# Optimization experiments

Measured on AMD Instinct MI355X. Metric: run time of the kernel, lower is better.

The kernel has to match this reference:

```python
import jax, jax.numpy as jnp
import numpy as np

N_NODES = 10000
N_EDGES = 320000
N_REL = 460
N_BASES = 30
D = 200


def setup_inputs() -> dict:
    key = jax.random.key(0)
    k = jax.random.split(key, 8)
    x = jax.random.normal(k[0], (N_NODES, D), dtype=jnp.float32)
    edge_index = jax.random.randint(k[1], (2, N_EDGES), 0, N_NODES, dtype=jnp.int32)
    edge_type = jax.random.randint(k[2], (N_EDGES,), 0, N_REL, dtype=jnp.int32)
    # Xavier-uniform-like init scales
    w_bound = float(np.sqrt(6.0 / (D + D)))
    c_bound = float(np.sqrt(6.0 / (N_REL + N_BASES)))
    weight = jax.random.uniform(k[3], (N_BASES, D, D), minval=-w_bound, maxval=w_bound, dtype=jnp.float32)
    coeff = jax.random.uniform(k[4], (N_REL, N_BASES), minval=-c_bound, maxval=c_bound, dtype=jnp.float32)
    self_weight = jax.random.uniform(k[5], (D, D), minval=-w_bound, maxval=w_bound, dtype=jnp.float32)
    bias = jnp.zeros((D,), dtype=jnp.float32)
    return {
        "x": x,
        "weight": weight,
        "coeff": coeff,
        "self_weight": self_weight,
        "bias": bias,
        "edge_index": edge_index,
        "edge_type": edge_type,
        "num_nodes": N_NODES,
    }


def reference(x, weight, coeff, self_weight, bias, edge_index, edge_type, num_nodes):
    # RelationalGraphConv.forward:
    #   W_r = sum_b coeff[r, b] * V_b ; msg_e = x[src_e] @ W_{type_e}
    #   out[n] = (sum_{e: tgt_e = n} msg_e) / max(in_deg[n], 1) + x @ W_self + bias
    src = edge_index[0]
    tgt = edge_index[1]
    src_feats = x[src]                    # (E, d_in) gather
    edge_coeff = coeff[edge_type]         # (E, B) gather

    # msg_e = sum_b coeff[type_e, b] * (src_e @ V_b): scan over bases to avoid
    # materializing an (E, B, d_out) intermediate (same math as W_r = coeff @ V).
    def body(acc, inputs):
        Vb, cb = inputs                   # (d_in, d_out), (E,)
        return acc + (src_feats @ Vb) * cb[:, None], None

    msg0 = jnp.zeros((src.shape[0], weight.shape[2]), dtype=x.dtype)
    msg, _ = jax.lax.scan(body, msg0, (weight, edge_coeff.T))  # (E, d_out)

    out = jax.ops.segment_sum(msg, tgt, num_segments=num_nodes)              # (N, d_out)
    deg = jax.ops.segment_sum(jnp.ones_like(tgt, dtype=x.dtype), tgt, num_segments=num_nodes)
    out = out / jnp.clip(deg, 1.0)[:, None]
    out = out + x @ self_weight + bias
    return out
```

## Files before the change

kernel.cpp:

```cpp
#include <hip/hip_runtime.h>
#include <hip/hip_bf16.h>

#define N_NODES 10000
#define N_EDGES 320000
#define N_REL   460
#define N_BASES 30
#define DIM     200
#define KZ      6016
#define KT      6240
#define NSTEPS  195
#define NTILES  157
#define NFRAG   16
#define KSPLIT  6
#define PROWS   10048
#define TKELEM  2048

#define PREP_B8 (NFRAG * NSTEPS * 64)
#define PREP_C  (N_REL * 16)
#define PREP_X8 (N_NODES * 28)
#define S1_TOTAL (N_EDGES + PREP_B8 + PREP_C)
#define S2_TOTAL (N_EDGES + PREP_X8)

using short8  = __attribute__((ext_vector_type(8))) short;
using s4v     = __attribute__((ext_vector_type(4))) short;
using floatx4 = __attribute__((ext_vector_type(4))) float;

__device__ __forceinline__ unsigned short f2bf(float f) {
    union { float f; unsigned u; } v; v.f = f;
    unsigned u = v.u;
    return (unsigned short)((u + 0x7fffu + ((u >> 16) & 1u)) >> 16);
}

__device__ __forceinline__ short8 pack8(const unsigned short* u) {
    union { unsigned short s[8]; short8 v; } p;
#pragma unroll
    for (int i = 0; i < 8; ++i) p.s[i] = u[i];
    return p.v;
}

__device__ __forceinline__ size_t asw_idx(int n, int c) {
    int t = n >> 6, sub = (n >> 4) & 3, rl = n & 15;
    int kk = c >> 5, w = c & 31;
    return (size_t)(t * NSTEPS + kk) * TKELEM + sub * 512 + rl * 32 + w;
}


__global__ void sort1_kernel(const int* __restrict__ tgt, int* __restrict__ deg,
                             const float* __restrict__ weight, const float* __restrict__ sw,
                             const float* __restrict__ coeff,
                             unsigned short* __restrict__ BSW, unsigned int* __restrict__ Cpair) {
    int idx = blockIdx.x * blockDim.x + threadIdx.x;
    if (idx < N_EDGES) {
        atomicAdd(&deg[tgt[idx]], 1);
        return;
    }
    idx -= N_EDGES;
    if (idx < PREP_B8) {
        int f = idx / (NSTEPS * 64);
        int rem = idx - f * (NSTEPS * 64);
        int kk = rem >> 6;
        int l = rem & 63;
        int rB = f * 16 + (l & 15);
        int kbase = kk * 32 + (l >> 4) * 8;
        unsigned short bs[8];
#pragma unroll
        for (int j = 0; j < 8; ++j) {
            int k = kbase + j;
            float v = 0.f;
            if (rB < DIM) {
                if (k < KZ) {
                    if (k < N_BASES * DIM) {
                        int b = k / DIM, kc = k - b * DIM;
                        v = weight[(b * DIM + kc) * DIM + rB];
                    }
                } else {
                    int jj = k - KZ;
                    if (jj < DIM) v = sw[jj * DIM + rB];
                }
            }
            bs[j] = f2bf(v);
        }
        *(short8*)(BSW + (size_t)idx * 8) = pack8(bs);
        return;
    }
    idx -= PREP_B8;
    if (idx < PREP_C) {
        int t = idx >> 4, m = idx & 15;
        unsigned lo = f2bf(coeff[t * N_BASES + m]);
        unsigned hi = (m + 16 < N_BASES) ? f2bf(coeff[t * N_BASES + m + 16]) : 0u;
        Cpair[idx] = lo | (hi << 16);
    }
}

__global__ __launch_bounds__(1024) void scan_kernel(const int* deg, int* starts,
                                                    int* cursor, float* dinv) {
    __shared__ int part[1024];
    int tid = threadIdx.x;
    const int PER = (N_NODES + 1023) / 1024;
    int base = tid * PER;
    int s = 0;
    for (int i = 0; i < PER; ++i) { int idx = base + i; if (idx < N_NODES) s += deg[idx]; }
    part[tid] = s; __syncthreads();
    for (int off = 1; off < 1024; off <<= 1) {
        int v = (tid >= off) ? part[tid - off] : 0;
        __syncthreads();
        part[tid] += v;
        __syncthreads();
    }
    int run = (tid > 0) ? part[tid - 1] : 0;
    for (int i = 0; i < PER; ++i) {
        int idx = base + i;
        if (idx < N_NODES) {
            int d = deg[idx];
            starts[idx] = run; cursor[idx] = run;
            dinv[idx] = 1.0f / (float)(d > 0 ? d : 1);
            run += d;
        }
    }
    if (tid == 1023) starts[N_NODES] = part[1023];
}


__global__ void sort2_kernel(const int* __restrict__ src, const int* __restrict__ tgt,
                             const int* __restrict__ etype, int* __restrict__ cursor,
                             int2* __restrict__ sedge,
                             const float* __restrict__ x, const int* __restrict__ deg,
                             unsigned short* __restrict__ XbfP, unsigned short* __restrict__ ASW) {
    int idx = blockIdx.x * blockDim.x + threadIdx.x;
    if (idx < N_EDGES) {
        int t = tgt[idx];
        int pos = atomicAdd(&cursor[t], 1);
        sedge[pos] = make_int2(src[idx], etype[idx]);
        return;
    }
    idx -= N_EDGES;
    if (idx < PREP_X8) {
        int n = idx / 28, t = idx - n * 28;
        int p = t >> 2, c4 = (t & 3) << 2;
        int cl = p * 32 + c4;
        int ch = cl + 16;
        int d = deg[n]; if (d < 1) d = 1;
        float df = (float)d;
        floatx4 vlo = (floatx4){0.f, 0.f, 0.f, 0.f};
        floatx4 vhi = (floatx4){0.f, 0.f, 0.f, 0.f};
        if (cl < DIM) vlo = *(const floatx4*)(x + (size_t)n * DIM + cl);
        if (ch < DIM) vhi = *(const floatx4*)(x + (size_t)n * DIM + ch);
        unsigned short xp[8], asl[4], ash[4];
#pragma unroll
        for (int i = 0; i < 4; ++i) {
            xp[2 * i]     = f2bf(vlo[i]);
            xp[2 * i + 1] = f2bf(vhi[i]);
            asl[i] = f2bf(df * vlo[i]);
            ash[i] = f2bf(df * vhi[i]);
        }
        *(short8*)(XbfP + (size_t)n * 224 + p * 32 + c4 * 2) = pack8(xp);
        union { unsigned short s[4]; s4v v; } ul, uh;
#pragma unroll
        for (int i = 0; i < 4; ++i) { ul.s[i] = asl[i]; uh.s[i] = ash[i]; }
        *(s4v*)(ASW + asw_idx(n, KZ + cl)) = ul.v;
        *(s4v*)(ASW + asw_idx(n, KZ + ch)) = uh.v;
    }
}


__global__ __launch_bounds__(256) void agg_kernel(const unsigned int* __restrict__ XbfP,
                                                  const unsigned int* __restrict__ Cpair,
                                                  const int* __restrict__ starts,
                                                  const int2* __restrict__ sedge,
                                                  unsigned short* __restrict__ ASW) {
    __shared__ __align__(16) unsigned short zbuf[4][3232];
    int lane = threadIdx.x & 63;
    int wave = threadIdx.x >> 6;
    int n = blockIdx.x * 4 + wave;
    int ln = lane & 15, q = lane >> 4;

    floatx4 acc0[13], acc1[13];
#pragma unroll
    for (int f = 0; f < 13; ++f) {
        acc0[f] = (floatx4){0.f, 0.f, 0.f, 0.f};
        acc1[f] = acc0[f];
    }

    int e0 = starts[n], e1 = starts[n + 1];
    for (int kb = e0; kb < e1; kb += 32) {
        int eb = kb + 8 * q;
        unsigned short a0v[8], a1v[8];
        int srcs[8];
#pragma unroll
        for (int j = 0; j < 8; ++j) {
            int e = eb + j;
            int ec = (e < e1) ? e : (e1 - 1);
            int2 sd = sedge[ec];
            unsigned cp = (e < e1) ? Cpair[sd.y * 16 + ln] : 0u;
            a0v[j] = (unsigned short)(cp & 0xffffu);
            a1v[j] = (unsigned short)(cp >> 16);
            srcs[j] = sd.x;
        }
        short8 A0 = pack8(a0v), A1 = pack8(a1v);

        unsigned pv[2][8];
#pragma unroll
        for (int j = 0; j < 8; ++j)
            pv[0][j] = XbfP[(size_t)srcs[j] * 112 + ln];
#pragma unroll
        for (int p = 0; p < 7; ++p) {
            int cur = p & 1, nxt = cur ^ 1;
            if (p < 6) {
#pragma unroll
                for (int j = 0; j < 8; ++j)
                    pv[nxt][j] = XbfP[(size_t)srcs[j] * 112 + (p + 1) * 16 + ln];
            }
            unsigned short lo[8], hi[8];
#pragma unroll
            for (int j = 0; j < 8; ++j) {
                lo[j] = (unsigned short)(pv[cur][j] & 0xffffu);
                hi[j] = (unsigned short)(pv[cur][j] >> 16);
            }
            short8 Blo = pack8(lo), Bhi = pack8(hi);
            int f0 = 2 * p;
            acc0[f0] = __builtin_amdgcn_mfma_f32_16x16x32_bf16(A0, Blo, acc0[f0], 0, 0, 0);
            acc1[f0] = __builtin_amdgcn_mfma_f32_16x16x32_bf16(A1, Blo, acc1[f0], 0, 0, 0);
            if (2 * p + 1 < 13) {
                acc0[2 * p + 1] = __builtin_amdgcn_mfma_f32_16x16x32_bf16(A0, Bhi, acc0[2 * p + 1], 0, 0, 0);
                acc1[2 * p + 1] = __builtin_amdgcn_mfma_f32_16x16x32_bf16(A1, Bhi, acc1[2 * p + 1], 0, 0, 0);
            }
        }
    }

    unsigned short* zb = zbuf[wave];
    int t = n >> 6, sub = (n >> 4) & 3, rl = n & 15;
    const uint4* zb4 = (const uint4*)zb;
    uint4* dst = (uint4*)ASW;
    size_t base_u4 = (size_t)t * NSTEPS * 256 + sub * 64 + rl * 4;

#pragma unroll
    for (int f = 0; f < 13; ++f) {
        int d = f * 16 + ln;
        if (d < DIM) {
#pragma unroll
            for (int i = 0; i < 4; ++i)
                zb[(q * 4 + i) * DIM + d] = f2bf(acc0[f][i]);
        }
    }
    for (int v = lane; v < 400; v += 64) {
        int kk = v >> 2, w8 = v & 3;
        dst[base_u4 + (size_t)kk * 256 + w8] = zb4[v];
    }

    if (lane < 16) zb[2800 + lane] = 0;
#pragma unroll
    for (int f = 0; f < 13; ++f) {
        int d = f * 16 + ln;
        if (d < DIM) {
#pragma unroll
            for (int i = 0; i < 4; ++i) {
                int b1 = 16 + q * 4 + i;
                if (b1 < N_BASES) zb[(b1 - 16) * DIM + d] = f2bf(acc1[f][i]);
            }
        }
    }
    for (int v = lane; v < 352; v += 64) {
        int kk = 100 + (v >> 2), w8 = v & 3;
        dst[base_u4 + (size_t)kk * 256 + w8] = zb4[v];
    }
}


#define GITER(VLIT, BU, BL, KK)                                                        \
  {                                                                                    \
    asm volatile("s_waitcnt vmcnt(" #VLIT ")" ::: "memory");                           \
    __builtin_amdgcn_sched_barrier(0);                                                 \
    asm volatile("s_barrier" ::: "memory");                                            \
    const int kk_ = (KK);                                                              \
    const int kld_ = (kk_ + 1 < ke) ? kk_ + 1 : ke - 1;                                \
    BL[0] = *(const short8*)(pb + ((size_t)(0 * 4 * NSTEPS) + kld_) * 512);            \
    BL[1] = *(const short8*)(pb + ((size_t)(1 * 4 * NSTEPS) + kld_) * 512);            \
    BL[2] = *(const short8*)(pb + ((size_t)(2 * 4 * NSTEPS) + kld_) * 512);            \
    BL[3] = *(const short8*)(pb + ((size_t)(3 * 4 * NSTEPS) + kld_) * 512);            \
    const int kst_ = (kk_ + 7 < ke) ? kk_ + 7 : ke - 1;                                \
    __builtin_amdgcn_global_load_lds(                                                  \
        (const unsigned int*)(aswt + (size_t)kst_ * TKELEM + goff),                    \
        (unsigned int*)(ldsw + ((kk_ + 7) & 7) * 2048), 16, 0, 0);                     \
    const unsigned short* sp_ = alds + (kk_ & 7) * 2048 + pread8;                      \
    short8 av0 = *(const short8*)(sp_);                                                \
    short8 av1 = *(const short8*)(sp_ + 512);                                          \
    short8 av2 = *(const short8*)(sp_ + 1024);                                         \
    short8 av3 = *(const short8*)(sp_ + 1536);                                         \
    _Pragma("unroll")                                                                  \
    for (int i_ = 0; i_ < 4; ++i_) {                                                   \
      acc[i_][0] = __builtin_amdgcn_mfma_f32_16x16x32_bf16(av0, BU[i_], acc[i_][0], 0, 0, 0); \
      acc[i_][1] = __builtin_amdgcn_mfma_f32_16x16x32_bf16(av1, BU[i_], acc[i_][1], 0, 0, 0); \
      acc[i_][2] = __builtin_amdgcn_mfma_f32_16x16x32_bf16(av2, BU[i_], acc[i_][2], 0, 0, 0); \
      acc[i_][3] = __builtin_amdgcn_mfma_f32_16x16x32_bf16(av3, BU[i_], acc[i_][3], 0, 0, 0); \
    }                                                                                  \
  }

__global__ __launch_bounds__(256, 4) void gemm_kernel(const unsigned short* __restrict__ ASW,
                                                      const unsigned short* __restrict__ BSW,
                                                      float* __restrict__ part) {
    __shared__ __align__(16) unsigned short alds[8 * 2048];
    int tid = threadIdx.x;
    int lane = tid & 63, wave = tid >> 6;
    int tile = blockIdx.x, chunk = blockIdx.y;
    int ks = (chunk * NSTEPS) / KSPLIT;
    int ke = ((chunk + 1) * NSTEPS) / KSPLIT;
    int ln = lane & 15, q = lane >> 4;

    const unsigned short* aswt = ASW + (size_t)tile * NSTEPS * TKELEM;
    const unsigned short* pb = BSW + (size_t)(wave * NSTEPS) * 512 + lane * 8;

    int gsw = (tid & 0xE0) | ((tid & 7) << 2) | ((tid >> 3) & 3);
    int goff = gsw * 8;
    int pread8 = ((((ln >> 3) & 1) << 5) | (q << 3) | (ln & 7)) * 8;
    unsigned short* ldsw = alds + wave * 512;

    floatx4 acc[4][4];
#pragma unroll
    for (int i = 0; i < 4; ++i)
#pragma unroll
        for (int s = 0; s < 4; ++s) acc[i][s] = (floatx4){0.f, 0.f, 0.f, 0.f};

    short8 bA[4], bB[4];

#pragma unroll
    for (int i = 0; i < 4; ++i)
        bA[i] = *(const short8*)(pb + ((size_t)(i * 4 * NSTEPS) + ks) * 512);
#pragma unroll
    for (int d = 0; d < 7; ++d)
        __builtin_amdgcn_global_load_lds(
            (const unsigned int*)(aswt + (size_t)(ks + d) * TKELEM + goff),
            (unsigned int*)(ldsw + ((ks + d) & 7) * 2048), 16, 0, 0);

    GITER(0,  bA, bB, ks + 0);
    GITER(5,  bB, bA, ks + 1);
    GITER(10, bA, bB, ks + 2);
    GITER(15, bB, bA, ks + 3);
    GITER(20, bA, bB, ks + 4);
    GITER(25, bB, bA, ks + 5);

    int kk = ks + 6;
    for (; kk + 1 < ke; kk += 2) {
        GITER(30, bA, bB, kk);
        GITER(30, bB, bA, kk + 1);
    }
    if (kk < ke) { GITER(30, bA, bB, kk); }

    int row0 = tile * 64;
    float* pbase = part + ((size_t)chunk * PROWS + row0) * 208;
#pragma unroll
    for (int i = 0; i < 4; ++i) {
        int fg = wave + 4 * i;
        if (fg < 13) {
            int c = fg * 16 + ln;
#pragma unroll
            for (int s = 0; s < 4; ++s)
#pragma unroll
                for (int ii = 0; ii < 4; ++ii)
                    pbase[(s * 16 + q * 4 + ii) * 208 + c] = acc[i][s][ii];
        }
    }
}


__global__ __launch_bounds__(256) void reduce_kernel(const float* __restrict__ part,
                                                     const float* __restrict__ dinv,
                                                     const float* __restrict__ bias,
                                                     float* __restrict__ out) {
    int idx = blockIdx.x * blockDim.x + threadIdx.x;
    if (idx >= N_NODES * 50) return;
    int r = idx / 50, cq = idx - r * 50;
    float4 s = {0.f, 0.f, 0.f, 0.f};
#pragma unroll
    for (int c = 0; c < KSPLIT; ++c) {
        float4 v = *(const float4*)(part + ((size_t)c * PROWS + r) * 208 + cq * 4);
        s.x += v.x; s.y += v.y; s.z += v.z; s.w += v.w;
    }
    float dv = dinv[r];
    float4 b = *(const float4*)(bias + cq * 4);
    float4 o;
    o.x = s.x * dv + b.x; o.y = s.y * dv + b.y;
    o.z = s.z * dv + b.z; o.w = s.w * dv + b.w;
    *(float4*)(out + (size_t)r * DIM + cq * 4) = o;
}


extern "C" void kernel_launch(void* const* d_in, const int* in_sizes, int n_in,
                              void* d_out, int out_size, void* d_ws, size_t ws_size,
                              hipStream_t stream) {
    const float* x      = (const float*)d_in[0];
    const float* weight = (const float*)d_in[1];
    const float* coeff  = (const float*)d_in[2];
    const float* selfw  = (const float*)d_in[3];
    const float* bias   = (const float*)d_in[4];
    const int*   eidx   = (const int*)d_in[5];
    const int*   etype  = (const int*)d_in[6];
    const int* src = eidx;
    const int* tgt = eidx + N_EDGES;
    float* out = (float*)d_out;

    char* ws = (char*)d_ws;
    size_t off = 0;
    auto carve = [&](size_t bytes) {
        char* p = ws + off;
        off += (bytes + 255) & ~(size_t)255;
        return p;
    };
    unsigned short* ASW  = (unsigned short*)carve((size_t)NTILES * NSTEPS * TKELEM * 2);
    unsigned short* BSW  = (unsigned short*)carve((size_t)NFRAG * NSTEPS * 512 * 2);
    float* part   = (float*)carve((size_t)KSPLIT * PROWS * 208 * 4);
    unsigned short* XbfP = (unsigned short*)carve((size_t)(N_NODES * 224 + 64) * 2);
    unsigned int*  Cpair = (unsigned int*)carve((size_t)N_REL * 16 * 4);
    int*   deg    = (int*)carve((size_t)N_NODES * 4);
    int*   starts = (int*)carve((size_t)(N_NODES + 1) * 4);
    int*   cursor = (int*)carve((size_t)N_NODES * 4);
    float* dinv   = (float*)carve((size_t)N_NODES * 4);
    int2*  sedge  = (int2*)carve((size_t)N_EDGES * 8);

    hipMemsetAsync(deg, 0, (size_t)N_NODES * 4, stream);

    sort1_kernel<<<(S1_TOTAL + 255) / 256, 256, 0, stream>>>(
        tgt, deg, weight, selfw, coeff, BSW, Cpair);

    scan_kernel<<<1, 1024, 0, stream>>>(deg, starts, cursor, dinv);

    sort2_kernel<<<(S2_TOTAL + 255) / 256, 256, 0, stream>>>(
        src, tgt, etype, cursor, sedge, x, deg, XbfP, ASW);

    agg_kernel<<<N_NODES / 4, 256, 0, stream>>>(
        (const unsigned int*)XbfP, Cpair, starts, sedge, ASW);

    dim3 ggrid(NTILES, KSPLIT);
    gemm_kernel<<<ggrid, 256, 0, stream>>>(ASW, BSW, part);

    reduce_kernel<<<(N_NODES * 50 + 255) / 256, 256, 0, stream>>>(part, dinv, bias, out);
}
```

Measured before the change: 254.7 us.

## Fuse memset, degree count, scan and edge sort into one cooperative kernel

Replaces the memset plus three separate preprocessing kernels (degree count/weight prep, prefix scan, edge bucketing/x prep) with a single cooperative kernel of 512 blocks that uses grid-wide syncs between phases. The aim is to remove several kernel launches and their inter-kernel gaps. In exchange, the scan now runs on 256 threads inside block 0 while every other block waits at the grid barrier. Grid-stride loops with a fixed grid may also use the machine less fully than the earlier one-thread-per-item launches.

```diff
diff --git a/kernel.cpp b/kernel.cpp
--- a/kernel.cpp
+++ b/kernel.cpp
@@ -1,5 +1,8 @@
 #include <hip/hip_runtime.h>
 #include <hip/hip_bf16.h>
+#include <hip/hip_cooperative_groups.h>
+
+namespace cg = cooperative_groups;
 
 #define N_NODES 10000
 #define N_EDGES 320000
@@ -18,8 +21,6 @@
 #define PREP_B8 (NFRAG * NSTEPS * 64)
 #define PREP_C  (N_REL * 16)
 #define PREP_X8 (N_NODES * 28)
-#define S1_TOTAL (N_EDGES + PREP_B8 + PREP_C)
-#define S2_TOTAL (N_EDGES + PREP_X8)
 
 using short8  = __attribute__((ext_vector_type(8))) short;
 using s4v     = __attribute__((ext_vector_type(4))) short;
@@ -45,19 +46,26 @@
 }
 
 
-__global__ void sort1_kernel(const int* __restrict__ tgt, int* __restrict__ deg,
-                             const float* __restrict__ weight, const float* __restrict__ sw,
-                             const float* __restrict__ coeff,
-                             unsigned short* __restrict__ BSW, unsigned int* __restrict__ Cpair) {
-    int idx = blockIdx.x * blockDim.x + threadIdx.x;
-    if (idx < N_EDGES) {
-        atomicAdd(&deg[tgt[idx]], 1);
-        return;
-    }
-    idx -= N_EDGES;
-    if (idx < PREP_B8) {
-        int f = idx / (NSTEPS * 64);
-        int rem = idx - f * (NSTEPS * 64);
+__global__ __launch_bounds__(256) void fused_sort_kernel(
+    const int* __restrict__ src, const int* __restrict__ tgt,
+    const int* __restrict__ etype,
+    const float* __restrict__ x, const float* __restrict__ weight,
+    const float* __restrict__ sw, const float* __restrict__ coeff,
+    int* deg, int* starts, int* cursor, float* dinv, int2* sedge,
+    unsigned short* __restrict__ XbfP, unsigned short* __restrict__ ASW,
+    unsigned short* __restrict__ BSW, unsigned int* __restrict__ Cpair)
+{
+    cg::grid_group grid = cg::this_grid();
+    int gsz = gridDim.x * blockDim.x;
+    int gid = blockIdx.x * blockDim.x + threadIdx.x;
+
+    for (int i = gid; i < N_NODES; i += gsz) deg[i] = 0;
+    grid.sync();
+
+    for (int i = gid; i < N_EDGES; i += gsz) atomicAdd(&deg[tgt[i]], 1);
+    for (int i = gid; i < PREP_B8; i += gsz) {
+        int f = i / (NSTEPS * 64);
+        int rem = i - f * (NSTEPS * 64);
         int kk = rem >> 6;
         int l = rem & 63;
         int rB = f * 16 + (l & 15);
@@ -80,62 +88,51 @@
             }
             bs[j] = f2bf(v);
         }
-        *(short8*)(BSW + (size_t)idx * 8) = pack8(bs);
-        return;
-    }
-    idx -= PREP_B8;
-    if (idx < PREP_C) {
-        int t = idx >> 4, m = idx & 15;
+        *(short8*)(BSW + (size_t)i * 8) = pack8(bs);
+    }
+    for (int i = gid; i < PREP_C; i += gsz) {
+        int t = i >> 4, m = i & 15;
         unsigned lo = f2bf(coeff[t * N_BASES + m]);
         unsigned hi = (m + 16 < N_BASES) ? f2bf(coeff[t * N_BASES + m + 16]) : 0u;
-        Cpair[idx] = lo | (hi << 16);
-    }
-}
-
-__global__ __launch_bounds__(1024) void scan_kernel(const int* deg, int* starts,
-                                                    int* cursor, float* dinv) {
-    __shared__ int part[1024];
-    int tid = threadIdx.x;
-    const int PER = (N_NODES + 1023) / 1024;
-    int base = tid * PER;
-    int s = 0;
-    for (int i = 0; i < PER; ++i) { int idx = base + i; if (idx < N_NODES) s += deg[idx]; }
-    part[tid] = s; __syncthreads();
-    for (int off = 1; off < 1024; off <<= 1) {
-        int v = (tid >= off) ? part[tid - off] : 0;
-        __syncthreads();
-        part[tid] += v;
-        __syncthreads();
-    }
-    int run = (tid > 0) ? part[tid - 1] : 0;
-    for (int i = 0; i < PER; ++i) {
-        int idx = base + i;
-        if (idx < N_NODES) {
-            int d = deg[idx];
-            starts[idx] = run; cursor[idx] = run;
-            dinv[idx] = 1.0f / (float)(d > 0 ? d : 1);
-            run += d;
-        }
-    }
-    if (tid == 1023) starts[N_NODES] = part[1023];
-}
-
-
-__global__ void sort2_kernel(const int* __restrict__ src, const int* __restrict__ tgt,
-                             const int* __restrict__ etype, int* __restrict__ cursor,
-                             int2* __restrict__ sedge,
-                             const float* __restrict__ x, const int* __restrict__ deg,
-                             unsigned short* __restrict__ XbfP, unsigned short* __restrict__ ASW) {
-    int idx = blockIdx.x * blockDim.x + threadIdx.x;
-    if (idx < N_EDGES) {
-        int t = tgt[idx];
+        Cpair[i] = lo | (hi << 16);
+    }
+    grid.sync();
+
+    if (blockIdx.x == 0) {
+        __shared__ int part2[256];
+        int tid = threadIdx.x;
+        const int PER = 40;
+        int base = tid * PER;
+        int s = 0;
+        for (int i = 0; i < PER; ++i) { int k = base + i; if (k < N_NODES) s += deg[k]; }
+        part2[tid] = s; __syncthreads();
+        for (int off = 1; off < 256; off <<= 1) {
+            int v = (tid >= off) ? part2[tid - off] : 0;
+            __syncthreads();
+            part2[tid] += v;
+            __syncthreads();
+        }
+        int run = (tid > 0) ? part2[tid - 1] : 0;
+        for (int i = 0; i < PER; ++i) {
+            int k = base + i;
+            if (k < N_NODES) {
+                int d = deg[k];
+                starts[k] = run; cursor[k] = run;
+                dinv[k] = 1.0f / (float)(d > 0 ? d : 1);
+                run += d;
+            }
+        }
+        if (tid == 255) starts[N_NODES] = part2[255];
+    }
+    grid.sync();
+
+    for (int i = gid; i < N_EDGES; i += gsz) {
+        int t = tgt[i];
         int pos = atomicAdd(&cursor[t], 1);
-        sedge[pos] = make_int2(src[idx], etype[idx]);
-        return;
-    }
-    idx -= N_EDGES;
-    if (idx < PREP_X8) {
-        int n = idx / 28, t = idx - n * 28;
+        sedge[pos] = make_int2(src[i], etype[i]);
+    }
+    for (int i = gid; i < PREP_X8; i += gsz) {
+        int n = i / 28, t = i - n * 28;
         int p = t >> 2, c4 = (t & 3) << 2;
         int cl = p * 32 + c4;
         int ch = cl + 16;
@@ -147,16 +144,16 @@
         if (ch < DIM) vhi = *(const floatx4*)(x + (size_t)n * DIM + ch);
         unsigned short xp[8], asl[4], ash[4];
 #pragma unroll
-        for (int i = 0; i < 4; ++i) {
-            xp[2 * i]     = f2bf(vlo[i]);
-            xp[2 * i + 1] = f2bf(vhi[i]);
-            asl[i] = f2bf(df * vlo[i]);
-            ash[i] = f2bf(df * vhi[i]);
+        for (int k = 0; k < 4; ++k) {
+            xp[2 * k]     = f2bf(vlo[k]);
+            xp[2 * k + 1] = f2bf(vhi[k]);
+            asl[k] = f2bf(df * vlo[k]);
+            ash[k] = f2bf(df * vhi[k]);
         }
         *(short8*)(XbfP + (size_t)n * 224 + p * 32 + c4 * 2) = pack8(xp);
         union { unsigned short s[4]; s4v v; } ul, uh;
 #pragma unroll
-        for (int i = 0; i < 4; ++i) { ul.s[i] = asl[i]; uh.s[i] = ash[i]; }
+        for (int k = 0; k < 4; ++k) { ul.s[k] = asl[k]; uh.s[k] = ash[k]; }
         *(s4v*)(ASW + asw_idx(n, KZ + cl)) = ul.v;
         *(s4v*)(ASW + asw_idx(n, KZ + ch)) = uh.v;
     }
@@ -416,15 +413,14 @@
     float* dinv   = (float*)carve((size_t)N_NODES * 4);
     int2*  sedge  = (int2*)carve((size_t)N_EDGES * 8);
 
-    hipMemsetAsync(deg, 0, (size_t)N_NODES * 4, stream);
-
-    sort1_kernel<<<(S1_TOTAL + 255) / 256, 256, 0, stream>>>(
-        tgt, deg, weight, selfw, coeff, BSW, Cpair);
-
-    scan_kernel<<<1, 1024, 0, stream>>>(deg, starts, cursor, dinv);
-
-    sort2_kernel<<<(S2_TOTAL + 255) / 256, 256, 0, stream>>>(
-        src, tgt, etype, cursor, sedge, x, deg, XbfP, ASW);
+    void* fargs[] = {
+        (void*)&src, (void*)&tgt, (void*)&etype,
+        (void*)&x, (void*)&weight, (void*)&selfw, (void*)&coeff,
+        (void*)&deg, (void*)&starts, (void*)&cursor, (void*)&dinv, (void*)&sedge,
+        (void*)&XbfP, (void*)&ASW, (void*)&BSW, (void*)&Cpair
+    };
+    hipLaunchCooperativeKernel((const void*)fused_sort_kernel,
+                               dim3(512), dim3(256), fargs, 0, stream);
 
     agg_kernel<<<N_NODES / 4, 256, 0, stream>>>(
         (const unsigned int*)XbfP, Cpair, starts, sedge, ASW);
```

Result: slower. 432.0 us (+69.6%).

## Store split-K partials in bf16, raise split to 8, shrink LDS ring to 4

Applied to the files above, without the earlier changes.

The split-K partial sums are now written as bf16 instead of fp32, which halves the partial-buffer traffic in both the GEMM epilogue and the reduce kernel. The K split rises from 6 to 8 chunks for more parallelism. The A-operand LDS ring shrinks from 8 to 4 stages with a shallower prefetch, which reduces shared memory per block and could raise occupancy but hides less latency. Rounding the partials to bf16 before summing adds error to the output.

```diff
diff --git a/kernel.cpp b/kernel.cpp
--- a/kernel.cpp
+++ b/kernel.cpp
@@ -11,7 +11,7 @@
 #define NSTEPS  195
 #define NTILES  157
 #define NFRAG   16
-#define KSPLIT  6
+#define KSPLIT  8
 #define PROWS   10048
 #define TKELEM  2048
 
@@ -29,6 +29,12 @@
     union { float f; unsigned u; } v; v.f = f;
     unsigned u = v.u;
     return (unsigned short)((u + 0x7fffu + ((u >> 16) & 1u)) >> 16);
+}
+
+__device__ __forceinline__ float bf2f(unsigned short s) {
+    union { unsigned u; float f; } v;
+    v.u = ((unsigned)s) << 16;
+    return v.f;
 }
 
 __device__ __forceinline__ short8 pack8(const unsigned short* u) {
@@ -277,11 +283,11 @@
     BL[1] = *(const short8*)(pb + ((size_t)(1 * 4 * NSTEPS) + kld_) * 512);            \
     BL[2] = *(const short8*)(pb + ((size_t)(2 * 4 * NSTEPS) + kld_) * 512);            \
     BL[3] = *(const short8*)(pb + ((size_t)(3 * 4 * NSTEPS) + kld_) * 512);            \
-    const int kst_ = (kk_ + 7 < ke) ? kk_ + 7 : ke - 1;                                \
+    const int kst_ = (kk_ + 3 < ke) ? kk_ + 3 : ke - 1;                                \
     __builtin_amdgcn_global_load_lds(                                                  \
         (const unsigned int*)(aswt + (size_t)kst_ * TKELEM + goff),                    \
-        (unsigned int*)(ldsw + ((kk_ + 7) & 7) * 2048), 16, 0, 0);                     \
-    const unsigned short* sp_ = alds + (kk_ & 7) * 2048 + pread8;                      \
+        (unsigned int*)(ldsw + ((kk_ + 3) & 3) * 2048), 16, 0, 0);                     \
+    const unsigned short* sp_ = alds + (kk_ & 3) * 2048 + pread8;                      \
     short8 av0 = *(const short8*)(sp_);                                                \
     short8 av1 = *(const short8*)(sp_ + 512);                                          \
     short8 av2 = *(const short8*)(sp_ + 1024);                                         \
@@ -297,8 +303,8 @@
 
 __global__ __launch_bounds__(256, 4) void gemm_kernel(const unsigned short* __restrict__ ASW,
                                                       const unsigned short* __restrict__ BSW,
-                                                      float* __restrict__ part) {
-    __shared__ __align__(16) unsigned short alds[8 * 2048];
+                                                      unsigned short* __restrict__ part) {
+    __shared__ __align__(16) unsigned short alds[4 * 2048];
     int tid = threadIdx.x;
     int lane = tid & 63, wave = tid >> 6;
     int tile = blockIdx.x, chunk = blockIdx.y;
@@ -326,27 +332,24 @@
     for (int i = 0; i < 4; ++i)
         bA[i] = *(const short8*)(pb + ((size_t)(i * 4 * NSTEPS) + ks) * 512);
 #pragma unroll
-    for (int d = 0; d < 7; ++d)
+    for (int d = 0; d < 3; ++d)
         __builtin_amdgcn_global_load_lds(
             (const unsigned int*)(aswt + (size_t)(ks + d) * TKELEM + goff),
-            (unsigned int*)(ldsw + ((ks + d) & 7) * 2048), 16, 0, 0);
-
-    GITER(0,  bA, bB, ks + 0);
-    GITER(5,  bB, bA, ks + 1);
-    GITER(10, bA, bB, ks + 2);
-    GITER(15, bB, bA, ks + 3);
-    GITER(20, bA, bB, ks + 4);
-    GITER(25, bB, bA, ks + 5);
-
-    int kk = ks + 6;
+            (unsigned int*)(ldsw + ((ks + d) & 3) * 2048), 16, 0, 0);
+
+    GITER(0, bA, bB, ks + 0);
+    GITER(4, bB, bA, ks + 1);
+    GITER(8, bA, bB, ks + 2);
+
+    int kk = ks + 3;
     for (; kk + 1 < ke; kk += 2) {
-        GITER(30, bA, bB, kk);
-        GITER(30, bB, bA, kk + 1);
-    }
-    if (kk < ke) { GITER(30, bA, bB, kk); }
+        GITER(8, bB, bA, kk);
+        GITER(8, bA, bB, kk + 1);
+    }
+    if (kk < ke) { GITER(8, bB, bA, kk); }
 
     int row0 = tile * 64;
-    float* pbase = part + ((size_t)chunk * PROWS + row0) * 208;
+    unsigned short* pbase = part + ((size_t)chunk * PROWS + row0) * 208;
 #pragma unroll
     for (int i = 0; i < 4; ++i) {
         int fg = wave + 4 * i;
@@ -356,30 +359,32 @@
             for (int s = 0; s < 4; ++s)
 #pragma unroll
                 for (int ii = 0; ii < 4; ++ii)
-                    pbase[(s * 16 + q * 4 + ii) * 208 + c] = acc[i][s][ii];
-        }
-    }
-}
-
-
-__global__ __launch_bounds__(256) void reduce_kernel(const float* __restrict__ part,
+                    pbase[(s * 16 + q * 4 + ii) * 208 + c] = f2bf(acc[i][s][ii]);
+        }
+    }
+}
+
+
+__global__ __launch_bounds__(256) void reduce_kernel(const unsigned short* __restrict__ part,
                                                      const float* __restrict__ dinv,
                                                      const float* __restrict__ bias,
                                                      float* __restrict__ out) {
     int idx = blockIdx.x * blockDim.x + threadIdx.x;
     if (idx >= N_NODES * 50) return;
     int r = idx / 50, cq = idx - r * 50;
-    float4 s = {0.f, 0.f, 0.f, 0.f};
+    float s0 = 0.f, s1 = 0.f, s2 = 0.f, s3 = 0.f;
 #pragma unroll
     for (int c = 0; c < KSPLIT; ++c) {
-        float4 v = *(const float4*)(part + ((size_t)c * PROWS + r) * 208 + cq * 4);
-        s.x += v.x; s.y += v.y; s.z += v.z; s.w += v.w;
+        union { unsigned short s[4]; s4v v; } u;
+        u.v = *(const s4v*)(part + ((size_t)c * PROWS + r) * 208 + cq * 4);
+        s0 += bf2f(u.s[0]); s1 += bf2f(u.s[1]);
+        s2 += bf2f(u.s[2]); s3 += bf2f(u.s[3]);
     }
     float dv = dinv[r];
     float4 b = *(const float4*)(bias + cq * 4);
     float4 o;
-    o.x = s.x * dv + b.x; o.y = s.y * dv + b.y;
-    o.z = s.z * dv + b.z; o.w = s.w * dv + b.w;
+    o.x = s0 * dv + b.x; o.y = s1 * dv + b.y;
+    o.z = s2 * dv + b.z; o.w = s3 * dv + b.w;
     *(float4*)(out + (size_t)r * DIM + cq * 4) = o;
 }
 
@@ -407,7 +412,7 @@
     };
     unsigned short* ASW  = (unsigned short*)carve((size_t)NTILES * NSTEPS * TKELEM * 2);
     unsigned short* BSW  = (unsigned short*)carve((size_t)NFRAG * NSTEPS * 512 * 2);
-    float* part   = (float*)carve((size_t)KSPLIT * PROWS * 208 * 4);
+    unsigned short* part = (unsigned short*)carve((size_t)KSPLIT * PROWS * 208 * 2);
     unsigned short* XbfP = (unsigned short*)carve((size_t)(N_NODES * 224 + 64) * 2);
     unsigned int*  Cpair = (unsigned int*)carve((size_t)N_REL * 16 * 4);
     int*   deg    = (int*)carve((size_t)N_NODES * 4);
```

New measurement: 247.8 us. 1.03x faster.
